# Kernel tuning notes

Measured on AMD Instinct MI355X. Metric: run time of the kernel, lower is better.

## Reference

```python
import jax, jax.numpy as jnp
import numpy as np

MARGIN = 0.1
CURV = 1.0
NUM_SAMPLES = 64        # num_samples_per_class
NUM_NEG = 8             # num_negatives
NUM_CLASSES = 128
EPS = 1e-7


def _time(x):
    # Lorentz time component from space components (MERU-style hyperboloid)
    return jnp.sqrt(1.0 / CURV + jnp.sum(x * x, axis=-1))


def _dist_from_inner(inner):
    # d(x,y) = (1/sqrt(c)) * acosh(-c * <x,y>_L), clamped for numerical safety
    return jnp.arccosh(jnp.clip(-CURV * inner, 1.0 + EPS, None)) / jnp.sqrt(CURV)


def pointwise_dist(x, y):
    inner = jnp.sum(x * y, axis=-1) - _time(x) * _time(y)   # [K]
    return _dist_from_inner(inner)


def pairwise_dist(x, y):
    inner = x @ y.T - _time(x)[:, None] * _time(y)[None, :]  # [K, C]
    return _dist_from_inner(inner)


def setup_inputs() -> dict:
    key = jax.random.key(0)
    k1, k2, k3 = jax.random.split(key, 3)
    voxel_emb = jax.random.normal(k1, (2, 64, 96, 96, 96), dtype=jnp.float32)
    labels = jax.random.randint(k2, (2, 96, 96, 96), 0, NUM_CLASSES, dtype=jnp.int32)
    label_emb = jax.random.normal(k3, (NUM_CLASSES, 64), dtype=jnp.float32)
    return {"voxel_emb": voxel_emb, "labels": labels, "label_emb": label_emb}


def reference(voxel_emb, labels, label_emb):
    B, D, H, W, Z = voxel_emb.shape
    C = label_emb.shape[0]
    voxel_flat = voxel_emb.transpose(0, 2, 3, 4, 1).reshape(-1, D)   # [N, D]
    labels_flat = labels.reshape(-1).astype(jnp.int32)               # [N]
    N = labels_flat.shape[0]

    key = jax.random.key(42)
    k_pri, k_neg = jax.random.split(key)

    # --- per-class random sampling via sort-by-(label, random priority) ---
    pri = jax.random.uniform(k_pri, (N,), dtype=jnp.float32)
    sort_key = labels_flat.astype(jnp.float32) * 2.0 + pri
    sorted_indices = jnp.argsort(sort_key)                # [N]
    sorted_labels = labels_flat[sorted_indices]           # [N], non-decreasing

    pos_in_sorted = jnp.arange(N, dtype=jnp.int32)
    first_occ = jax.ops.segment_min(pos_in_sorted, sorted_labels,
                                    num_segments=C)       # [C]
    positions = pos_in_sorted - first_occ[sorted_labels]  # rank within class
    sample_mask = positions < NUM_SAMPLES                 # keep first NUM_SAMPLES per class

    # scatter sampled voxel indices into fixed [C * NUM_SAMPLES] slots (jit-safe K)
    Kmax = C * NUM_SAMPLES
    slot = jnp.where(sample_mask, sorted_labels * NUM_SAMPLES + positions, Kmax)
    sampled_idx = jnp.zeros(Kmax + 1, jnp.int32).at[slot].set(sorted_indices)[:Kmax]
    valid = jnp.zeros(Kmax + 1, bool).at[slot].set(True)[:Kmax]       # [Kmax]
    sampled_classes = jnp.arange(Kmax, dtype=jnp.int32) // NUM_SAMPLES

    anchors = voxel_flat[sampled_idx]          # [Kmax, D]
    positives = label_emb[sampled_classes]     # [Kmax, D]

    d_pos = pointwise_dist(anchors, positives)        # [Kmax]
    all_dists = pairwise_dist(anchors, label_emb)     # [Kmax, C]

    # --- random negative class selection (exclude true class) ---
    neg_mask = jnp.arange(C)[None, :] != sampled_classes[:, None]
    neg_scores = jax.random.uniform(k_neg, (Kmax, C), dtype=jnp.float32)
    neg_scores = jnp.where(neg_mask, neg_scores, -1.0)
    n_neg = min(NUM_NEG, C - 1)
    _, neg_indices = jax.lax.top_k(neg_scores, n_neg)           # [Kmax, n_neg]
    d_neg = jnp.take_along_axis(all_dists, neg_indices, axis=1)

    triplet = jnp.maximum(MARGIN + d_pos[:, None] - d_neg, 0.0)  # [Kmax, n_neg]
    vf = valid.astype(triplet.dtype)
    loss = jnp.sum(triplet * vf[:, None]) / jnp.maximum(jnp.sum(vf) * n_neg, 1.0)
    return loss
```

## Files before the change

kernel.cpp:

```cpp
#include <hip/hip_runtime.h>
#include <stdint.h>
#include <stddef.h>


#define JAX_PARTITIONABLE 1

static constexpr int C_CLASSES = 128;
static constexpr int NSAMP     = 64;
static constexpr int KMAX      = C_CLASSES * NSAMP;
static constexpr int NNEG      = 8;
static constexpr int DIM       = 64;
static constexpr int SPATIAL   = 96 * 96 * 96;
static constexpr int NTOT      = 2 * SPATIAL;
static constexpr int SH        = 16;
static constexpr int SLOT      = 64;
static constexpr int CSORT     = 512;
#define THRESH 0.02f

__host__ __device__ __forceinline__ void tf2x32(uint32_t k0, uint32_t k1,
                                                uint32_t x0, uint32_t x1,
                                                uint32_t& o0, uint32_t& o1) {
  uint32_t ks2 = k0 ^ k1 ^ 0x1BD11BDAu;
  x0 += k0; x1 += k1;
#define TF_R(r) { x0 += x1; x1 = (x1 << (r)) | (x1 >> (32 - (r))); x1 ^= x0; }
  TF_R(13) TF_R(15) TF_R(26) TF_R(6)
  x0 += k1;  x1 += ks2 + 1u;
  TF_R(17) TF_R(29) TF_R(16) TF_R(24)
  x0 += ks2; x1 += k0 + 2u;
  TF_R(13) TF_R(15) TF_R(26) TF_R(6)
  x0 += k0;  x1 += k1 + 3u;
  TF_R(17) TF_R(29) TF_R(16) TF_R(24)
  x0 += k1;  x1 += ks2 + 4u;
  TF_R(13) TF_R(15) TF_R(26) TF_R(6)
  x0 += ks2; x1 += k0 + 5u;
#undef TF_R
  o0 = x0; o1 = x1;
}

__device__ __forceinline__ uint32_t jax_bits_at(uint32_t k0, uint32_t k1,
                                                uint32_t i, uint32_t half) {
  uint32_t o0, o1;
#if JAX_PARTITIONABLE
  (void)half;
  tf2x32(k0, k1, 0u, i, o0, o1);
  return o0 ^ o1;
#else
  if (i < half) { tf2x32(k0, k1, i, i + half, o0, o1); return o0; }
  tf2x32(k0, k1, i - half, i, o0, o1); return o1;
#endif
}

__device__ __forceinline__ float jax_uniform(uint32_t bits) {
  return __uint_as_float((bits >> 9) | 0x3F800000u) - 1.0f;
}

__device__ __forceinline__ uint32_t f32_orderable(float f) {
  uint32_t u = __float_as_uint(f);
  return (u & 0x80000000u) ? ~u : (u | 0x80000000u);
}

__device__ __forceinline__ unsigned long long umin64(unsigned long long a,
                                                     unsigned long long b) {
  return (a < b) ? a : b;
}

__device__ unsigned int       g_cnt[C_CLASSES * SH];
__device__ unsigned long long g_cand[C_CLASSES * SH * SLOT];
__device__ double             g_loss_accum;
__device__ int                g_valid_total;

__global__ void k_init() {
  int t = threadIdx.x;
  for (int i = t; i < C_CLASSES * SH; i += 256) g_cnt[i] = 0u;
  if (t == 0) { g_loss_accum = 0.0; g_valid_total = 0; }
}

__global__ void k_gather(const int* __restrict__ labels,
                         uint32_t pk0, uint32_t pk1) {
  int i = blockIdx.x * blockDim.x + threadIdx.x;
  if (i >= NTOT) return;
  uint32_t bits = jax_bits_at(pk0, pk1, (uint32_t)i, (uint32_t)(NTOT / 2));
  float u = jax_uniform(bits);
  int lab = labels[i];
  if ((unsigned)lab >= (unsigned)C_CLASSES) return;
  if (u < THRESH) {
    float skey = (float)lab * 2.0f + u;
    int shard = i & (SH - 1);
    unsigned cell = (unsigned)(lab * SH + shard);
    unsigned pos = atomicAdd(&g_cnt[cell], 1u);
    if (pos < (unsigned)SLOT) {
      g_cand[cell * SLOT + pos] =
          ((unsigned long long)__float_as_uint(skey) << 32) | (unsigned)i;
    }
  }
}

__global__ void __launch_bounds__(256)
k_class(const float* __restrict__ voxel, const float* __restrict__ lemb,
        uint32_t nk0, uint32_t nk1) {
  __shared__ unsigned long long sh[CSORT];
  __shared__ float Lsh[C_CLASSES][DIM + 1];
  __shared__ float Ash[NSAMP][DIM + 1];
  __shared__ float tL[C_CLASSES];
  __shared__ float tA[NSAMP];
  __shared__ int   sidx[NSAMP];
  __shared__ int   s_nv;
  __shared__ unsigned s_pf[SH];
  __shared__ unsigned s_ct[SH];
  __shared__ double red[256];

  const int c0  = blockIdx.x;
  const int tid = threadIdx.x;

  for (int i = tid; i < CSORT; i += 256) sh[i] = 0xFFFFFFFFFFFFFFFFULL;
  for (int i = tid; i < C_CLASSES * DIM; i += 256)
    Lsh[i >> 6][i & 63] = lemb[i];
  __syncthreads();

  if (tid == 0) {
    unsigned acc = 0;
    for (int s = 0; s < SH; ++s) {
      unsigned c = g_cnt[c0 * SH + s];
      if (c > (unsigned)SLOT) c = SLOT;
      if (acc + c > (unsigned)CSORT) c = CSORT - acc;
      s_pf[s] = acc; s_ct[s] = c; acc += c;
    }
    s_nv = (int)((acc < (unsigned)NSAMP) ? acc : (unsigned)NSAMP);
  }
  __syncthreads();

  for (int s = 0; s < SH; ++s) {
    unsigned base = s_pf[s], ct = s_ct[s];
    for (unsigned j = tid; j < ct; j += 256)
      sh[base + j] = g_cand[(c0 * SH + s) * SLOT + j];
  }
  __syncthreads();

  for (unsigned k = 2; k <= (unsigned)CSORT; k <<= 1) {
    for (unsigned j = k >> 1; j > 0; j >>= 1) {
      for (unsigned i = tid; i < (unsigned)CSORT; i += 256) {
        unsigned ixj = i ^ j;
        if (ixj > i) {
          unsigned long long a = sh[i], b = sh[ixj];
          bool up = ((i & k) == 0);
          bool sw = up ? (a > b) : (a < b);
          if (sw) { sh[i] = b; sh[ixj] = a; }
        }
      }
      __syncthreads();
    }
  }

  if (tid < NSAMP) {
    bool v = tid < s_nv;
    sidx[tid] = v ? (int)(unsigned)(sh[tid] & 0xFFFFFFFFull) : 0;
  }
  if (tid == 0) atomicAdd(&g_valid_total, s_nv);
  __syncthreads();

  for (int i = tid; i < NSAMP * DIM; i += 256) {
    int r = i >> 6, d = i & 63;
    int n = sidx[r];
    int b = n / SPATIAL;
    int s = n - b * SPATIAL;
    Ash[r][d] = voxel[(size_t)(b * DIM + d) * (size_t)SPATIAL + (size_t)s];
  }
  __syncthreads();

  if (tid < C_CLASSES) {
    float sum = 0.0f;
#pragma unroll
    for (int d = 0; d < DIM; ++d) { float v = Lsh[tid][d]; sum += v * v; }
    tL[tid] = sqrtf(1.0f + sum);
  } else if (tid < C_CLASSES + NSAMP) {
    int r = tid - C_CLASSES;
    float sum = 0.0f;
#pragma unroll
    for (int d = 0; d < DIM; ++d) { float v = Ash[r][d]; sum += v * v; }
    tA[r] = sqrtf(1.0f + sum);
  }
  __syncthreads();

  float contrib = 0.0f;
  if (tid < NSAMP) {
    const int r = tid;
    const int k = c0 * NSAMP + r;
    unsigned long long s0 = 0, s1 = 1, s2 = 2, s3 = 3,
                       s4 = 4, s5 = 5, s6 = 6, s7 = 7;
    for (int c = 0; c < C_CLASSES; ++c) {
      uint32_t m = (uint32_t)(k * C_CLASSES + c);
      uint32_t bits = jax_bits_at(nk0, nk1, m, (uint32_t)(KMAX * C_CLASSES / 2));
      float v = (c == c0) ? -1.0f : jax_uniform(bits);
      unsigned long long key =
          ((unsigned long long)f32_orderable(v) << 32) | (unsigned)(127 - c);
      unsigned long long w = umin64(umin64(umin64(s0, s1), umin64(s2, s3)),
                                    umin64(umin64(s4, s5), umin64(s6, s7)));
      if (key > w) {
        s0 = (s0 == w) ? key : s0;  s1 = (s1 == w) ? key : s1;
        s2 = (s2 == w) ? key : s2;  s3 = (s3 == w) ? key : s3;
        s4 = (s4 == w) ? key : s4;  s5 = (s5 == w) ? key : s5;
        s6 = (s6 == w) ? key : s6;  s7 = (s7 == w) ? key : s7;
      }
    }
    float dp;
    {
      float sum = 0.0f;
#pragma unroll
      for (int d = 0; d < DIM; ++d) sum = fmaf(Ash[r][d], Lsh[c0][d], sum);
      float inner = sum - tA[r] * tL[c0];
      dp = acoshf(fmaxf(-inner, 1.0000001192092896f));
    }
    float ssum = 0.0f;
#define TAKE(S) { int c_ = 127 - (int)((S) & 0xFFFFFFFFull); \
                  float sum_ = 0.0f; \
                  _Pragma("unroll") \
                  for (int d = 0; d < DIM; ++d) \
                    sum_ = fmaf(Ash[r][d], Lsh[c_][d], sum_); \
                  float inner_ = sum_ - tA[r] * tL[c_]; \
                  float dn_ = acoshf(fmaxf(-inner_, 1.0000001192092896f)); \
                  ssum += fmaxf(0.1f + dp - dn_, 0.0f); }
    TAKE(s0) TAKE(s1) TAKE(s2) TAKE(s3) TAKE(s4) TAKE(s5) TAKE(s6) TAKE(s7)
#undef TAKE
    contrib = (r < s_nv) ? ssum : 0.0f;
  }

  red[tid] = (double)contrib;
  __syncthreads();
  for (int off = 128; off > 0; off >>= 1) {
    if (tid < off) red[tid] += red[tid + off];
    __syncthreads();
  }
  if (tid == 0) atomicAdd(&g_loss_accum, red[0]);
}

__global__ void k_final(float* __restrict__ out) {
  double denom = (double)g_valid_total * (double)NNEG;
  if (denom < 1.0) denom = 1.0;
  out[0] = (float)(g_loss_accum / denom);
}

extern "C" void kernel_launch(void* const* d_in, const int* in_sizes, int n_in,
                              void* d_out, int out_size, void* d_ws, size_t ws_size,
                              hipStream_t stream) {
  (void)in_sizes; (void)n_in; (void)out_size; (void)d_ws; (void)ws_size;
  const float* voxel  = (const float*)d_in[0];
  const int*   labels = (const int*)d_in[1];
  const float* lemb   = (const float*)d_in[2];
  float*       out    = (float*)d_out;

  uint32_t pk0, pk1, nk0, nk1;
#if JAX_PARTITIONABLE
  tf2x32(0u, 42u, 0u, 0u, pk0, pk1);
  tf2x32(0u, 42u, 0u, 1u, nk0, nk1);
#else
  uint32_t a0, a1, b0, b1;
  tf2x32(0u, 42u, 0u, 2u, a0, b0);
  tf2x32(0u, 42u, 1u, 3u, a1, b1);
  pk0 = a0; pk1 = a1; nk0 = b0; nk1 = b1;
#endif

  k_init<<<1, 256, 0, stream>>>();
  k_gather<<<NTOT / 256, 256, 0, stream>>>(labels, pk0, pk1);
  k_class<<<C_CLASSES, 256, 0, stream>>>(voxel, lemb, nk0, nk1);
  k_final<<<1, 1, 0, stream>>>(out);
}
```

Baseline: 585.3 us.

## Spread gather atomics over more padded shards and parallelize candidate compaction

Raises the shard count per class from 16 to 64 and pads each atomic counter onto its own cache line, which reduces atomic contention and false sharing in the gather kernel. The per-class prefix computation in k_class becomes a parallel shared-memory scan, and candidate copying is spread over one thread per shard instead of a serial loop. Slots per shard shrink from 64 to 32, so a shard can overflow more easily. Counter memory grows, and k_init now launches multiple blocks to zero the padded counters.

```diff
diff --git a/kernel.cpp b/kernel.cpp
--- a/kernel.cpp
+++ b/kernel.cpp
@@ -12,9 +12,10 @@
 static constexpr int DIM       = 64;
 static constexpr int SPATIAL   = 96 * 96 * 96;
 static constexpr int NTOT      = 2 * SPATIAL;
-static constexpr int SH        = 16;
-static constexpr int SLOT      = 64;
+static constexpr int SH        = 64;
+static constexpr int SLOT      = 32;
 static constexpr int CSORT     = 512;
+static constexpr int CNT_PAD   = 16;
 #define THRESH 0.02f
 
 __host__ __device__ __forceinline__ void tf2x32(uint32_t k0, uint32_t k1,
@@ -64,15 +65,15 @@
   return (a < b) ? a : b;
 }
 
-__device__ unsigned int       g_cnt[C_CLASSES * SH];
+__device__ unsigned int       g_cnt[C_CLASSES * SH * CNT_PAD];
 __device__ unsigned long long g_cand[C_CLASSES * SH * SLOT];
 __device__ double             g_loss_accum;
 __device__ int                g_valid_total;
 
 __global__ void k_init() {
-  int t = threadIdx.x;
-  for (int i = t; i < C_CLASSES * SH; i += 256) g_cnt[i] = 0u;
-  if (t == 0) { g_loss_accum = 0.0; g_valid_total = 0; }
+  int i = blockIdx.x * blockDim.x + threadIdx.x;
+  if (i < C_CLASSES * SH) g_cnt[i * CNT_PAD] = 0u;
+  if (i == 0) { g_loss_accum = 0.0; g_valid_total = 0; }
 }
 
 __global__ void k_gather(const int* __restrict__ labels,
@@ -87,7 +88,7 @@
     float skey = (float)lab * 2.0f + u;
     int shard = i & (SH - 1);
     unsigned cell = (unsigned)(lab * SH + shard);
-    unsigned pos = atomicAdd(&g_cnt[cell], 1u);
+    unsigned pos = atomicAdd(&g_cnt[cell * CNT_PAD], 1u);
     if (pos < (unsigned)SLOT) {
       g_cand[cell * SLOT + pos] =
           ((unsigned long long)__float_as_uint(skey) << 32) | (unsigned)i;
@@ -107,6 +108,7 @@
   __shared__ int   s_nv;
   __shared__ unsigned s_pf[SH];
   __shared__ unsigned s_ct[SH];
+  __shared__ unsigned s_scan[SH];
   __shared__ double red[256];
 
   const int c0  = blockIdx.x;
@@ -115,24 +117,37 @@
   for (int i = tid; i < CSORT; i += 256) sh[i] = 0xFFFFFFFFFFFFFFFFULL;
   for (int i = tid; i < C_CLASSES * DIM; i += 256)
     Lsh[i >> 6][i & 63] = lemb[i];
-  __syncthreads();
-
+
+  if (tid < SH) {
+    unsigned c = g_cnt[(c0 * SH + tid) * CNT_PAD];
+    if (c > (unsigned)SLOT) c = SLOT;
+    s_ct[tid] = c;
+    s_scan[tid] = c;
+  }
+  __syncthreads();
+
+#pragma unroll
+  for (int off = 1; off < SH; off <<= 1) {
+    unsigned v = 0;
+    if (tid < SH && tid >= off) v = s_scan[tid - off];
+    __syncthreads();
+    if (tid < SH) s_scan[tid] += v;
+    __syncthreads();
+  }
+  if (tid < SH) s_pf[tid] = s_scan[tid] - s_ct[tid];
   if (tid == 0) {
-    unsigned acc = 0;
-    for (int s = 0; s < SH; ++s) {
-      unsigned c = g_cnt[c0 * SH + s];
-      if (c > (unsigned)SLOT) c = SLOT;
-      if (acc + c > (unsigned)CSORT) c = CSORT - acc;
-      s_pf[s] = acc; s_ct[s] = c; acc += c;
-    }
-    s_nv = (int)((acc < (unsigned)NSAMP) ? acc : (unsigned)NSAMP);
-  }
-  __syncthreads();
-
-  for (int s = 0; s < SH; ++s) {
-    unsigned base = s_pf[s], ct = s_ct[s];
-    for (unsigned j = tid; j < ct; j += 256)
-      sh[base + j] = g_cand[(c0 * SH + s) * SLOT + j];
+    unsigned total = s_scan[SH - 1];
+    if (total > (unsigned)CSORT) total = CSORT;
+    s_nv = (int)((total < (unsigned)NSAMP) ? total : (unsigned)NSAMP);
+  }
+  __syncthreads();
+
+  if (tid < SH) {
+    unsigned base = s_pf[tid], ct = s_ct[tid];
+    if (base > (unsigned)CSORT) base = CSORT;
+    if (base + ct > (unsigned)CSORT) ct = CSORT - base;
+    for (unsigned j = 0; j < ct; ++j)
+      sh[base + j] = g_cand[(c0 * SH + tid) * SLOT + j];
   }
   __syncthreads();
 
@@ -259,7 +274,7 @@
   pk0 = a0; pk1 = a1; nk0 = b0; nk1 = b1;
 #endif
 
-  k_init<<<1, 256, 0, stream>>>();
+  k_init<<<(C_CLASSES * SH + 255) / 256, 256, 0, stream>>>();
   k_gather<<<NTOT / 256, 256, 0, stream>>>(labels, pk0, pk1);
   k_class<<<C_CLASSES, 256, 0, stream>>>(voxel, lemb, nk0, nk1);
   k_final<<<1, 1, 0, stream>>>(out);
```

Measured after the change: 579.8 us. Within noise of the previous version (-0.9%).
